# Optimization experiments

Hardware: AMD Instinct MI355X
Metric: run time of the kernel (lower is better)

Reference implementation:

```python
import jax, jax.numpy as jnp
import numpy as np

HIDDEN = 2048
N_HEADS = 32
HEAD_DIM = HIDDEN // N_HEADS  # 64
SEQ = 2048
BATCH = 1
CHUNK = 256
TOPK = 4
THETA = 10000.0
EPS = 1e-6
NEG = jnp.float32(-1e30)


def setup_inputs() -> dict:
    key = jax.random.key(0)
    ks = jax.random.split(key, 8)
    s = 0.02
    return {
        "hidden_states": jax.random.normal(ks[0], (BATCH, SEQ, HIDDEN), jnp.float32),
        "Wq": jax.random.normal(ks[1], (HIDDEN, HIDDEN), jnp.float32) * s,
        "Wk": jax.random.normal(ks[2], (HIDDEN, HIDDEN), jnp.float32) * s,
        "Wv": jax.random.normal(ks[3], (HIDDEN, HIDDEN), jnp.float32) * s,
        "Wo": jax.random.normal(ks[4], (HIDDEN, HIDDEN), jnp.float32) * s,
        "Wg1": jax.random.normal(ks[5], (HEAD_DIM, HIDDEN), jnp.float32) * s,
        "Wg2": jax.random.normal(ks[6], (HIDDEN, HEAD_DIM), jnp.float32) * s,
        "o_norm_weight": jnp.ones((HEAD_DIM,), jnp.float32),
    }


def _rope(t):
    # t: [B, S, H, D]; non-interleaved (NeoX-style) rotary over full head dim
    D = t.shape[-1]
    pos = jnp.arange(t.shape[1], dtype=jnp.float32)
    inv_freq = 1.0 / (THETA ** (jnp.arange(0, D, 2, dtype=jnp.float32) / D))
    freqs = pos[:, None] * inv_freq[None, :]            # [S, D/2]
    cos = jnp.cos(freqs)[None, :, None, :]
    sin = jnp.sin(freqs)[None, :, None, :]
    t1, t2 = t[..., : D // 2], t[..., D // 2:]
    return jnp.concatenate([t1 * cos - t2 * sin, t1 * sin + t2 * cos], axis=-1)


def reference(hidden_states, Wq, Wk, Wv, Wo, Wg1, Wg2, o_norm_weight):
    B, S, _ = hidden_states.shape
    H, D, C = N_HEADS, HEAD_DIM, CHUNK
    NC = S // C

    q = (hidden_states @ Wq.T).reshape(B, S, H, D)
    k = (hidden_states @ Wk.T).reshape(B, S, H, D)
    v = (hidden_states @ Wv.T).reshape(B, S, H, D)
    q, k = _rope(q), _rope(k)

    # --- MoBA gating: per-chunk mean-pooled keys scored against each query ---
    kmean = k.reshape(B, NC, C, H, D).mean(axis=2)           # [B, NC, H, D]
    gate = jnp.einsum('bshd,bnhd->bhsn', q, kmean)           # [B, H, S, NC]

    pos = jnp.arange(S)
    q_chunk = pos // C                                       # [S]
    chunk_ids = jnp.arange(NC)
    future = chunk_ids[None, :] > q_chunk[:, None]           # [S, NC]
    self_blk = chunk_ids[None, :] == q_chunk[:, None]
    gate = jnp.where(future[None, None], NEG, gate)
    gate = jnp.where(self_blk[None, None], -NEG, gate)       # self block always selected

    _, topk_idx = jax.lax.top_k(gate, TOPK)                  # [B, H, S, TOPK]
    sel = jax.nn.one_hot(topk_idx, NC, dtype=jnp.bool_).any(axis=-2)  # [B, H, S, NC]

    # --- block-sparse causal attention over selected chunks ---
    allowed = jnp.take(sel, q_chunk, axis=-1)                # [B, H, S, S] key j -> chunk j//C
    causal = pos[None, :] <= pos[:, None]                    # [S, S]
    allowed = allowed & causal[None, None]

    scale = 1.0 / np.sqrt(D)
    scores = jnp.einsum('bshd,bthd->bhst', q, k) * scale
    scores = jnp.where(allowed, scores, NEG)
    p = jax.nn.softmax(scores, axis=-1)
    o = jnp.einsum('bhst,bthd->bshd', p, v)                  # [B, S, H, D]

    # --- gated RMSNorm (FusedRMSNormGated, sigmoid activation) ---
    g = ((hidden_states @ Wg1.T) @ Wg2.T).reshape(B, S, H, D)
    rms = jax.lax.rsqrt(jnp.mean(o * o, axis=-1, keepdims=True) + EPS)
    o = o * rms * o_norm_weight * jax.nn.sigmoid(g)

    return (o.reshape(B, S, H * D)) @ Wo.T
```

## Files before the change

kernel.cpp:

```cpp
#include <hip/hip_runtime.h>
#include <hip/hip_bf16.h>


typedef __attribute__((ext_vector_type(8))) short s8v;
typedef __attribute__((ext_vector_type(4))) float f4v;

#define MFMA16(A,B,C) __builtin_amdgcn_mfma_f32_16x16x32_bf16(A,B,C,0,0,0)

__device__ __forceinline__ unsigned short f2b_rne(float f){
  unsigned u = __builtin_bit_cast(unsigned, f);
  u = (u + 0x7FFFu + ((u>>16)&1u)) >> 16;
  return (unsigned short)u;
}
__device__ __forceinline__ float b2f(unsigned short h){
  unsigned u = ((unsigned)h)<<16;
  return __builtin_bit_cast(float, u);
}
__device__ __forceinline__ unsigned pack2(float a, float b){
  return (unsigned)f2b_rne(a) | ((unsigned)f2b_rne(b)<<16);
}
__device__ __forceinline__ void gld16(const void* g, void* l){
  __builtin_amdgcn_global_load_lds((const __attribute__((address_space(1))) void*)g,
                                   (__attribute__((address_space(3))) void*)l, 16, 0, 0);
}

__global__ __launch_bounds__(256) void rtab_k(double2* __restrict__ tab){
  const int i = blockIdx.x*256 + threadIdx.x;
  if (i >= 2048*32) return;
  const int d2 = i & 31, s = i >> 5;
  const double invf = 1.0 / pow(10000.0, (double)d2 / 32.0);
  const double ph = (double)s * invf;
  tab[i] = make_double2(cos(ph), sin(ph));
}

__global__ __launch_bounds__(256) void f2b4_k(const float* __restrict__ s,
                                              unsigned short* __restrict__ d, int n4){
  int i = blockIdx.x*256 + threadIdx.x;
  if (i >= n4) return;
  const float4 v = *(const float4*)(s + (size_t)i*4);
  uint2 p; p.x = pack2(v.x, v.y); p.y = pack2(v.z, v.w);
  *(uint2*)(d + (size_t)i*4) = p;
}

__global__ __launch_bounds__(256) void f2bs_k(const float* __restrict__ s,
    unsigned short* __restrict__ hi, unsigned short* __restrict__ lo, int n4){
  int i = blockIdx.x*256 + threadIdx.x;
  if (i >= n4) return;
  const float4 v = *(const float4*)(s + (size_t)i*4);
  unsigned short h0 = f2b_rne(v.x), h1 = f2b_rne(v.y), h2 = f2b_rne(v.z), h3 = f2b_rne(v.w);
  uint2 ph; ph.x = (unsigned)h0 | ((unsigned)h1<<16); ph.y = (unsigned)h2 | ((unsigned)h3<<16);
  uint2 pl; pl.x = pack2(v.x - b2f(h0), v.y - b2f(h1));
  pl.y = pack2(v.z - b2f(h2), v.w - b2f(h3));
  *(uint2*)(hi + (size_t)i*4) = ph;
  *(uint2*)(lo + (size_t)i*4) = pl;
}

__global__ __launch_bounds__(256) void d2bs_k(const double* __restrict__ s,
    unsigned short* __restrict__ hi, unsigned short* __restrict__ lo, int n2){
  const int i = blockIdx.x*256 + threadIdx.x;
  if (i >= n2) return;
  #pragma unroll
  for (int j = 0; j < 2; ++j) {
    const float f = (float)s[(size_t)i*2+j];
    const unsigned short h = f2b_rne(f);
    hi[(size_t)i*2+j] = h;
    lo[(size_t)i*2+j] = f2b_rne(f - b2f(h));
  }
}

__global__ __launch_bounds__(1024) void wsum_k(const float* __restrict__ hs,
    const double2* __restrict__ tab, double* __restrict__ Ac, double* __restrict__ As){
  const int n = blockIdx.x, d2 = blockIdx.y, tid = threadIdx.x;
  double ac0=0, as0=0, ac1=0, as1=0;
  for (int i = 0; i < 256; ++i) {
    const int s = n*256 + i;
    const double2 t = tab[s*32 + d2];
    const double v0 = (double)hs[(size_t)s*2048 + tid];
    const double v1 = (double)hs[(size_t)s*2048 + tid + 1024];
    ac0 += t.x*v0; as0 += t.y*v0;
    ac1 += t.x*v1; as1 += t.y*v1;
  }
  const size_t ro = (size_t)(n*32 + d2)*2048;
  Ac[ro + tid]      = ac0*(1.0/256.0);
  Ac[ro + tid+1024] = ac1*(1.0/256.0);
  As[ro + tid]      = as0*(1.0/256.0);
  As[ro + tid+1024] = as1*(1.0/256.0);
}

__global__ __launch_bounds__(256) void kmcomb_k(const float* __restrict__ Cc,
    const float* __restrict__ Cs, double* __restrict__ Km){
  const int i = blockIdx.x*256 + threadIdx.x;
  const int d = i & 63, h = (i>>6) & 31, n = i >> 11;
  const int d2 = d & 31;
  const size_t row = (size_t)(n*32 + d2)*2048;
  double v;
  if (d < 32) v = (double)Cc[row + h*64 + d2] - (double)Cs[row + h*64 + d2 + 32];
  else        v = (double)Cs[row + h*64 + d2] + (double)Cc[row + h*64 + d2 + 32];
  Km[(size_t)(n*32 + h)*64 + d] = v;
}

__global__ __launch_bounds__(256) void gate_topk_k(const float* __restrict__ Qf,
    const double* __restrict__ Km, unsigned char* __restrict__ Allow,
    unsigned char* __restrict__ Flags){
  const int h = blockIdx.x, c = blockIdx.y, t = threadIdx.x;
  __shared__ double km[512];
  km[t]     = Km[((t>>6)*32 + h)*64 + (t&63)];
  km[t+256] = Km[(((t+256)>>6)*32 + h)*64 + (t&63)];
  __syncthreads();
  const int s = c*256 + t;
  const float* qp = Qf + (size_t)s*2048 + h*64;
  double g[8] = {};
  for (int d = 0; d < 64; ++d) {
    const double qv = (double)qp[d];
    #pragma unroll
    for (int n2 = 0; n2 < 8; ++n2) g[n2] += qv*km[n2*64+d];
  }
  double margin = 1e300;
  if (c >= 4) {
    unsigned pm = 0;
    double v[4];
    for (int rep = 0; rep < 4; ++rep) {
      double best = -1e308; int bi = 0;
      #pragma unroll
      for (int n2 = 0; n2 < 8; ++n2) {
        const bool take = (n2 < c) && !((pm>>n2)&1u) && (g[n2] > best);
        best = take ? g[n2] : best;
        bi   = take ? n2 : bi;
      }
      v[rep] = best; pm |= 1u<<bi;
    }
    margin = v[2] - v[3];
  }
  Flags[h*2048 + s] = (margin < 1e-3) ? 1 : 0;
  #pragma unroll
  for (int n2 = 0; n2 < 8; ++n2) if (n2 > c) g[n2] = -1e300;
  g[c] = 1e300;
  unsigned mask = 0;
  for (int rep = 0; rep < 4; ++rep) {
    double best = -1e308; int bi = 0;
    #pragma unroll
    for (int n2 = 0; n2 < 8; ++n2) {
      const bool take = !((mask>>n2)&1u) && (g[n2] > best);
      best = take ? g[n2] : best;
      bi   = take ? n2 : bi;
    }
    mask |= 1u<<bi;
  }
  Allow[h*2048 + s] = (unsigned char)mask;
}

__global__ __launch_bounds__(64) void repair_k(
    const float* __restrict__ hs, const float* __restrict__ Wq,
    const double2* __restrict__ tab, const double* __restrict__ Km,
    const unsigned char* __restrict__ Flags, unsigned char* __restrict__ Allow)
{
  const int s = blockIdx.x, d = threadIdx.x;
  __shared__ double qr[64];
  __shared__ double g8[8];
  for (int h = 0; h < 32; ++h) {
    if (!Flags[h*2048 + s]) continue;
    const float* hrow = hs + (size_t)s*2048;
    const float* wrow = Wq + (size_t)(h*64 + d)*2048;
    double a0=0,a1=0,a2=0,a3=0;
    for (int k = 0; k < 2048; k += 4) {
      a0 += (double)hrow[k]  *(double)wrow[k];
      a1 += (double)hrow[k+1]*(double)wrow[k+1];
      a2 += (double)hrow[k+2]*(double)wrow[k+2];
      a3 += (double)hrow[k+3]*(double)wrow[k+3];
    }
    qr[d] = (a0+a1)+(a2+a3);
    __syncthreads();
    const double2 t = tab[s*32 + (d&31)];
    const double rot = (d < 32) ? (qr[d]*t.x - qr[d+32]*t.y)
                                : (qr[d-32]*t.y + qr[d]*t.x);
    __syncthreads();
    qr[d] = rot;
    __syncthreads();
    if (d < 8) {
      double g = 0;
      const double* kmp = Km + (size_t)(d*32 + h)*64;
      for (int dd = 0; dd < 64; ++dd) g += qr[dd]*kmp[dd];
      g8[d] = g;
    }
    __syncthreads();
    if (d == 0) {
      const int c = s >> 8;
      double g[8];
      #pragma unroll
      for (int n2 = 0; n2 < 8; ++n2)
        g[n2] = (n2 > c) ? -1e300 : ((n2 == c) ? 1e300 : g8[n2]);
      unsigned mask = 0;
      for (int rep = 0; rep < 4; ++rep) {
        double best = -1e308; int bi = 0;
        #pragma unroll
        for (int n2 = 0; n2 < 8; ++n2) {
          const bool take = !((mask>>n2)&1u) && (g[n2] > best);
          best = take ? g[n2] : best;
          bi   = take ? n2 : bi;
        }
        mask |= 1u<<bi;
      }
      Allow[h*2048 + s] = (unsigned char)mask;
    }
    __syncthreads();
  }
}

__global__ __launch_bounds__(256) void gemm4_bt(
    const unsigned short* __restrict__ Ah, const unsigned short* __restrict__ Al,
    const unsigned short* __restrict__ Bh, const unsigned short* __restrict__ Bl,
    float* __restrict__ C, int M, int N, int K)
{
  alignas(16) __shared__ char SAh[16384];
  alignas(16) __shared__ char SAl[16384];
  alignas(16) __shared__ char SBh[16384];
  alignas(16) __shared__ char SBl[16384];
  const int t = threadIdx.x;
  const int wave = t>>6, lane = t&63, lg = lane>>4, lr = lane&15;
  const int wm = wave >> 1, wn = wave & 1;
  const int m0 = blockIdx.x*128, n0 = blockIdx.y*128;
  const unsigned short* Ahb = Ah + (size_t)m0*K;
  const unsigned short* Alb = Al + (size_t)m0*K;
  const unsigned short* Bhb = Bh + (size_t)n0*K;
  const unsigned short* Blb = Bl + (size_t)n0*K;
  f4v acc[4][4] = {};
  #pragma unroll 1
  for (int kt = 0; kt < K; kt += 64) {
    __syncthreads();
    #pragma unroll
    for (int i = 0; i < 4; ++i) {
      const size_t go = (size_t)(i*32 + (t>>3))*K + kt + (t&7)*8;
      gld16(Ahb + go, SAh + i*4096 + wave*1024);
      gld16(Alb + go, SAl + i*4096 + wave*1024);
      gld16(Bhb + go, SBh + i*4096 + wave*1024);
      gld16(Blb + go, SBl + i*4096 + wave*1024);
    }
    __syncthreads();
    #pragma unroll
    for (int kk = 0; kk < 2; ++kk) {
      s8v ah[4], al[4], bh[4], bl[4];
      #pragma unroll
      for (int i = 0; i < 4; ++i) {
        const int ro = (wm*64 + i*16 + lr)*128 + kk*64 + lg*16;
        ah[i] = *(const s8v*)&SAh[ro];
        al[i] = *(const s8v*)&SAl[ro];
      }
      #pragma unroll
      for (int j = 0; j < 4; ++j) {
        const int ro = (wn*64 + j*16 + lr)*128 + kk*64 + lg*16;
        bh[j] = *(const s8v*)&SBh[ro];
        bl[j] = *(const s8v*)&SBl[ro];
      }
      #pragma unroll
      for (int i = 0; i < 4; ++i)
        #pragma unroll
        for (int j = 0; j < 4; ++j) {
          f4v a = acc[i][j];
          a = MFMA16(ah[i], bh[j], a);
          a = MFMA16(ah[i], bl[j], a);
          a = MFMA16(al[i], bh[j], a);
          a = MFMA16(al[i], bl[j], a);
          acc[i][j] = a;
        }
    }
  }
  #pragma unroll
  for (int i = 0; i < 4; ++i)
    #pragma unroll
    for (int j = 0; j < 4; ++j) {
      const int row = m0 + wm*64 + i*16 + lg*4;
      const int col = n0 + wn*64 + j*16 + lr;
      #pragma unroll
      for (int r = 0; r < 4; ++r)
        C[(size_t)(row+r)*N + col] = acc[i][j][r];
    }
}

template<int BM, int BN, int WN, bool OUTBF>
__global__ __launch_bounds__(256) void gemm_bt(
    const unsigned short* __restrict__ A, const unsigned short* __restrict__ B,
    void* __restrict__ C, int M, int N, int K)
{
  alignas(16) __shared__ char AsB[BM*128];
  alignas(16) __shared__ char BsB[BN*128];
  const int t = threadIdx.x;
  const int wave = t>>6, lane = t&63, lg = lane>>4, lr = lane&15;
  const int wm = wave / WN, wn = wave % WN;
  const int m0 = blockIdx.x*BM, n0 = blockIdx.y*BN;
  const unsigned short* Ab = A + (size_t)m0*K;
  const unsigned short* Bb = B + (size_t)n0*K;
  f4v acc[4][4] = {};
  #pragma unroll 1
  for (int kt = 0; kt < K; kt += 64) {
    __syncthreads();
    #pragma unroll
    for (int i = 0; i < BM/32; ++i)
      gld16(Ab + (size_t)(i*32 + (t>>3))*K + kt + (t&7)*8, AsB + i*4096 + wave*1024);
    #pragma unroll
    for (int i = 0; i < BN/32; ++i)
      gld16(Bb + (size_t)(i*32 + (t>>3))*K + kt + (t&7)*8, BsB + i*4096 + wave*1024);
    __syncthreads();
    #pragma unroll
    for (int kk = 0; kk < 2; ++kk) {
      s8v af[4], bfr[4];
      #pragma unroll
      for (int i = 0; i < 4; ++i)
        af[i] = *(const s8v*)&AsB[(wm*64 + i*16 + lr)*128 + kk*64 + lg*16];
      #pragma unroll
      for (int j = 0; j < 4; ++j)
        bfr[j] = *(const s8v*)&BsB[(wn*64 + j*16 + lr)*128 + kk*64 + lg*16];
      #pragma unroll
      for (int i = 0; i < 4; ++i)
        #pragma unroll
        for (int j = 0; j < 4; ++j)
          acc[i][j] = MFMA16(af[i], bfr[j], acc[i][j]);
    }
  }
  #pragma unroll
  for (int i = 0; i < 4; ++i)
    #pragma unroll
    for (int j = 0; j < 4; ++j) {
      const int row = m0 + wm*64 + i*16 + lg*4;
      const int col = n0 + wn*64 + j*16 + lr;
      #pragma unroll
      for (int r = 0; r < 4; ++r) {
        if (OUTBF) ((unsigned short*)C)[(size_t)(row+r)*N + col] = f2b_rne(acc[i][j][r]);
        else       ((float*)C)[(size_t)(row+r)*N + col] = acc[i][j][r];
      }
    }
}

__global__ __launch_bounds__(256) void rope32q_k(float* __restrict__ Qf,
    unsigned short* __restrict__ Qb, const double2* __restrict__ tab){
  const int idx = blockIdx.x*256 + threadIdx.x;
  const int d2 = idx & 31, hh = (idx>>5)&31, s = idx>>10;
  const double2 t = tab[s*32 + d2];
  const float cs = (float)t.x, sn = (float)t.y;
  const size_t base = (size_t)s*2048 + hh*64 + d2;
  const float q1 = Qf[base], q2 = Qf[base+32];
  const float o1 = q1*cs - q2*sn, o2 = q1*sn + q2*cs;
  Qf[base] = o1; Qf[base+32] = o2;
  Qb[base] = f2b_rne(o1); Qb[base+32] = f2b_rne(o2);
}

__global__ __launch_bounds__(256) void rope32_k(const float* __restrict__ Kf,
    unsigned short* __restrict__ Kb, const double2* __restrict__ tab){
  const int idx = blockIdx.x*256 + threadIdx.x;
  const int d2 = idx & 31, hh = (idx>>5)&31, s = idx>>10;
  const double2 t = tab[s*32 + d2];
  const float cs = (float)t.x, sn = (float)t.y;
  const size_t base = (size_t)s*2048 + hh*64 + d2;
  const float k1 = Kf[base], k2 = Kf[base+32];
  Kb[base]    = f2b_rne(k1*cs - k2*sn);
  Kb[base+32] = f2b_rne(k1*sn + k2*cs);
}

__global__ __launch_bounds__(256) void vtrans_k(const float* __restrict__ V,
                                                unsigned short* __restrict__ Vt){
  __shared__ unsigned short tile[64][68];
  const int s0 = blockIdx.x*64, c0 = blockIdx.y*64;
  const int tx = threadIdx.x & 63, ty = threadIdx.x >> 6;
  #pragma unroll
  for (int rr = 0; rr < 16; ++rr) {
    const int r = ty*16 + rr;
    tile[tx][r] = f2b_rne(V[(size_t)(s0+r)*2048 + c0+tx]);
  }
  __syncthreads();
  #pragma unroll
  for (int rr = 0; rr < 16; ++rr) {
    const int cc = ty*16 + rr;
    Vt[(size_t)(c0+cc)*2048 + s0+tx] = tile[cc][tx];
  }
}

__global__ __launch_bounds__(64) void attn_k(
    const unsigned short* __restrict__ Qb, const unsigned short* __restrict__ Kb,
    const unsigned short* __restrict__ Vt, const float* __restrict__ Gf,
    const unsigned char* __restrict__ Allow, const float* __restrict__ Wn,
    float* __restrict__ Of)
{
  const int h = blockIdx.x, c = blockIdx.y, zb = blockIdx.z;
  const int lane = threadIdx.x, lg = lane>>4, lr = lane&15;
  const int qbase = c*256 + zb*16;
  alignas(16) __shared__ char P[2048];

  const size_t qrow = (size_t)(qbase + lr);
  const s8v qf0 = *(const s8v*)&Qb[qrow*2048 + h*64 + lg*8];
  const s8v qf1 = *(const s8v*)&Qb[qrow*2048 + h*64 + 32 + lg*8];
  const unsigned am = Allow[h*2048 + qrow];
  const int q = qbase + lr;
  const int sw = (lr&7)<<4;

  float mx = -1e30f, ls = 0.f;
  f4v ot[4] = {};

  for (int n = 0; n <= c; ++n) {
    if (!__ballot((am>>n)&1u)) continue;
    const int okc = (am>>n)&1;
    #pragma unroll 1
    for (int t4 = 0; t4 < 4; ++t4) {
      const int kb0 = n*256 + t4*64;
      s8v kf[4][2];
      #pragma unroll
      for (int i = 0; i < 4; ++i) {
        const size_t krow = (size_t)(kb0 + i*16 + lr);
        kf[i][0] = *(const s8v*)&Kb[krow*2048 + h*64 + lg*8];
        kf[i][1] = *(const s8v*)&Kb[krow*2048 + h*64 + 32 + lg*8];
      }
      f4v st[4];
      #pragma unroll
      for (int i = 0; i < 4; ++i) {
        f4v zz = {};
        zz = MFMA16(kf[i][0], qf0, zz);
        st[i] = MFMA16(kf[i][1], qf1, zz);
      }
      float cm = -__builtin_inff();
      #pragma unroll
      for (int i = 0; i < 4; ++i)
        #pragma unroll
        for (int r = 0; r < 4; ++r) {
          float v = st[i][r]*0.125f;
          const int key = kb0 + i*16 + lg*4 + r;
          const bool ok = okc && (n != c || key <= q);
          v = ok ? v : -__builtin_inff();
          st[i][r] = v;
          cm = fmaxf(cm, v);
        }
      cm = fmaxf(cm, __shfl_xor(cm, 16));
      cm = fmaxf(cm, __shfl_xor(cm, 32));
      const float nm = fmaxf(mx, cm);
      const float al = __expf(mx - nm);
      mx = nm;
      float ps = 0.f;
      #pragma unroll
      for (int i = 0; i < 4; ++i) {
        const float p0 = __expf(st[i][0]-mx);
        const float p1 = __expf(st[i][1]-mx);
        const float p2 = __expf(st[i][2]-mx);
        const float p3 = __expf(st[i][3]-mx);
        ps += (p0+p1)+(p2+p3);
        uint2 pk; pk.x = pack2(p0,p1); pk.y = pack2(p2,p3);
        *(uint2*)&P[lr*128 + ((i*32 + lg*8) ^ sw)] = pk;
      }
      ps += __shfl_xor(ps, 16);
      ps += __shfl_xor(ps, 32);
      ls = ls*al + ps;
      #pragma unroll
      for (int jd = 0; jd < 4; ++jd) ot[jd] *= al;
      asm volatile("s_waitcnt lgkmcnt(0)" ::: "memory");
      __builtin_amdgcn_sched_barrier(0);
      #pragma unroll
      for (int kk = 0; kk < 2; ++kk) {
        s8v vfr[4];
        #pragma unroll
        for (int jd = 0; jd < 4; ++jd)
          vfr[jd] = *(const s8v*)&Vt[(size_t)(h*64 + jd*16 + lr)*2048 + kb0 + kk*32 + lg*8];
        const s8v pfr = *(const s8v*)&P[lr*128 + ((kk*64 + lg*16) ^ sw)];
        #pragma unroll
        for (int jd = 0; jd < 4; ++jd)
          ot[jd] = MFMA16(vfr[jd], pfr, ot[jd]);
      }
      asm volatile("s_waitcnt lgkmcnt(0)" ::: "memory");
      __builtin_amdgcn_sched_barrier(0);
    }
  }
  const float inv_ = 1.0f/ls;
  float ssum = 0.f;
  #pragma unroll
  for (int jd = 0; jd < 4; ++jd)
    #pragma unroll
    for (int r = 0; r < 4; ++r) {
      const float o = ot[jd][r]*inv_;
      ot[jd][r] = o;
      ssum += o*o;
    }
  ssum += __shfl_xor(ssum, 16);
  ssum += __shfl_xor(ssum, 32);
  const float rmsv = rsqrtf(ssum*(1.0f/64.0f) + 1e-6f);
  #pragma unroll
  for (int jd = 0; jd < 4; ++jd) {
    const float4 w4 = *(const float4*)&Wn[jd*16 + lg*4];
    const float4 g4 = *(const float4*)&Gf[qrow*2048 + h*64 + jd*16 + lg*4];
    float4 o4;
    o4.x = ot[jd][0]*rmsv*w4.x*(1.0f/(1.0f+__expf(-g4.x)));
    o4.y = ot[jd][1]*rmsv*w4.y*(1.0f/(1.0f+__expf(-g4.y)));
    o4.z = ot[jd][2]*rmsv*w4.z*(1.0f/(1.0f+__expf(-g4.z)));
    o4.w = ot[jd][3]*rmsv*w4.w*(1.0f/(1.0f+__expf(-g4.w)));
    *(float4*)&Of[qrow*2048 + h*64 + jd*16 + lg*4] = o4;
  }
}

extern "C" void kernel_launch(void* const* d_in, const int* in_sizes, int n_in,
                              void* d_out, int out_size, void* d_ws, size_t ws_size,
                              hipStream_t stream)
{
  const float* hs  = (const float*)d_in[0];
  const float* Wq  = (const float*)d_in[1];
  const float* Wk  = (const float*)d_in[2];
  const float* Wv  = (const float*)d_in[3];
  const float* Wo  = (const float*)d_in[4];
  const float* Wg1 = (const float*)d_in[5];
  const float* Wg2 = (const float*)d_in[6];
  const float* Wn  = (const float*)d_in[7];

  const size_t S2 = (size_t)2048*2048;
  const size_t MB = (size_t)1<<20;
  char* ws = (char*)d_ws;
  double2*        tab   = (double2*)       (ws);
  unsigned short* Wg1b  = (unsigned short*)(ws + 1*MB);
  unsigned short* Wg2b  = (unsigned short*)(ws + 1*MB + 262144);
  unsigned short* g1b   = (unsigned short*)(ws + 1*MB + 524288);
  double*         km    = (double*)        (ws + 1*MB + 786432);
  unsigned char*  allow = (unsigned char*) (ws + 1*MB + 917504);
  unsigned char*  flags = (unsigned char*) (ws + 1*MB + 983040);
  unsigned short* hsh   = (unsigned short*)(ws + 2*MB);
  unsigned short* hsl   = (unsigned short*)(ws + 10*MB);
  unsigned short* Wqh   = (unsigned short*)(ws + 18*MB);
  unsigned short* Wql   = (unsigned short*)(ws + 26*MB);
  unsigned short* Wkh   = (unsigned short*)(ws + 34*MB);
  unsigned short* Wkl   = (unsigned short*)(ws + 42*MB);
  unsigned short* Wvb   = (unsigned short*)(ws + 50*MB);
  float*          qf    = (float*)         (ws + 58*MB);
  float*          kf    = (float*)         (ws + 74*MB);
  float*          vf    = (float*)         (ws + 90*MB);
  double*         Ac    = (double*)        (ws + 106*MB);
  double*         As    = (double*)        (ws + 110*MB);
  unsigned short* Ach   = (unsigned short*)(ws + 18*MB);
  unsigned short* Acl   = (unsigned short*)(ws + 19*MB);
  unsigned short* Ash   = (unsigned short*)(ws + 20*MB);
  unsigned short* Asl   = (unsigned short*)(ws + 21*MB);
  float*          Cc    = (float*)         (ws + 22*MB);
  float*          Cs    = (float*)         (ws + 24*MB);
  unsigned short* qb    = (unsigned short*)(ws + 26*MB);
  unsigned short* kb    = (unsigned short*)(ws + 42*MB);
  unsigned short* vt    = (unsigned short*)(ws + 74*MB);
  unsigned short* ofb   = (unsigned short*)(ws + 82*MB);
  float*          gf    = (float*)         (ws + 90*MB);
  float*          of    = (float*)         (ws + 58*MB);
  unsigned short* Wob   = (unsigned short*)(ws + 106*MB);
  (void)ws_size; (void)in_sizes; (void)n_in; (void)out_size;

  rtab_k<<<256,256,0,stream>>>(tab);
  f2bs_k<<<4096,256,0,stream>>>(hs, hsh, hsl, (int)(S2/4));
  f2bs_k<<<4096,256,0,stream>>>(Wq, Wqh, Wql, (int)(S2/4));
  f2bs_k<<<4096,256,0,stream>>>(Wk, Wkh, Wkl, (int)(S2/4));
  f2b4_k<<<4096,256,0,stream>>>(Wv, Wvb, (int)(S2/4));
  f2b4_k<<<128,256,0,stream>>>(Wg1, Wg1b, 64*2048/4);
  f2b4_k<<<128,256,0,stream>>>(Wg2, Wg2b, 2048*64/4);

  gemm4_bt<<<dim3(16,16),256,0,stream>>>(hsh, hsl, Wqh, Wql, qf, 2048, 2048, 2048);
  gemm_bt<128,128,2,false><<<dim3(16,16),256,0,stream>>>(hsh, Wkh, kf, 2048, 2048, 2048);
  gemm_bt<128,128,2,false><<<dim3(16,16),256,0,stream>>>(hsh, Wvb, vf, 2048, 2048, 2048);

  rope32q_k<<<8192,256,0,stream>>>(qf, qb, tab);

  wsum_k<<<dim3(8,32),1024,0,stream>>>(hs, tab, Ac, As);
  d2bs_k<<<1024,256,0,stream>>>(Ac, Ach, Acl, 262144);
  d2bs_k<<<1024,256,0,stream>>>(As, Ash, Asl, 262144);
  gemm4_bt<<<dim3(2,16),256,0,stream>>>(Ach, Acl, Wkh, Wkl, Cc, 256, 2048, 2048);
  gemm4_bt<<<dim3(2,16),256,0,stream>>>(Ash, Asl, Wkh, Wkl, Cs, 256, 2048, 2048);
  kmcomb_k<<<64,256,0,stream>>>(Cc, Cs, km);

  rope32_k<<<8192,256,0,stream>>>(kf, kb, tab);

  gate_topk_k<<<dim3(32,8),256,0,stream>>>(qf, km, allow, flags);
  repair_k<<<2048,64,0,stream>>>(hs, Wq, tab, km, flags, allow);

  vtrans_k<<<dim3(32,32),256,0,stream>>>(vf, vt);
  gemm_bt<256,64,1,true><<<dim3(8,1),256,0,stream>>>(hsh, Wg1b, g1b, 2048, 64, 2048);
  gemm_bt<128,128,2,false><<<dim3(16,16),256,0,stream>>>(g1b, Wg2b, gf, 2048, 2048, 64);

  attn_k<<<dim3(32,8,16),64,0,stream>>>(qb, kb, vt, gf, allow, Wn, of);

  f2b4_k<<<4096,256,0,stream>>>(of, ofb, (int)(S2/4));
  f2b4_k<<<4096,256,0,stream>>>(Wo, Wob, (int)(S2/4));
  gemm_bt<128,128,2,false><<<dim3(16,16),256,0,stream>>>(ofb, Wob, d_out, 2048, 2048, 2048);
}
```

Before: 850.4 us.

## Software-pipeline K loads with double buffering and hoist V loads in sparse attention

Restructures the block-sparse attention loop to precompute a bitmask of active chunks and iterate over them directly. K fragments for the next 64-key tile, including the first tile of the next active chunk, are prefetched into alternating register buffers while the current tile is computed. V fragments are now loaded at the start of each tile rather than after the softmax, so global-load latency can overlap the QK MFMAs and the softmax. The cost is higher register pressure from the extra K buffer and the hoisted V fragments, which may reduce occupancy.

Result: no change. 837.1 us (-1.6%).

```diff
diff --git a/kernel.cpp b/kernel.cpp
--- a/kernel.cpp
+++ b/kernel.cpp
@@ -394,74 +394,97 @@
   float mx = -1e30f, ls = 0.f;
   f4v ot[4] = {};
 
-  for (int n = 0; n <= c; ++n) {
-    if (!__ballot((am>>n)&1u)) continue;
-    const int okc = (am>>n)&1;
-    #pragma unroll 1
-    for (int t4 = 0; t4 < 4; ++t4) {
-      const int kb0 = n*256 + t4*64;
-      s8v kf[4][2];
-      #pragma unroll
-      for (int i = 0; i < 4; ++i) {
-        const size_t krow = (size_t)(kb0 + i*16 + lr);
-        kf[i][0] = *(const s8v*)&Kb[krow*2048 + h*64 + lg*8];
-        kf[i][1] = *(const s8v*)&Kb[krow*2048 + h*64 + 32 + lg*8];
+  unsigned act = 0;
+  for (int n = 0; n <= c; ++n)
+    if (__ballot((am>>n)&1u)) act |= (1u<<n);
+
+  auto loadK = [&](s8v (&kf)[4][2], int kb0){
+    #pragma unroll
+    for (int i = 0; i < 4; ++i) {
+      const size_t krow = (size_t)(kb0 + i*16 + lr);
+      kf[i][0] = *(const s8v*)&Kb[krow*2048 + h*64 + lg*8];
+      kf[i][1] = *(const s8v*)&Kb[krow*2048 + h*64 + 32 + lg*8];
+    }
+  };
+
+  if (act) {
+    int n = (int)__builtin_ctz(act);
+    s8v kA[4][2], kB[4][2];
+    loadK(kA, n*256);
+    while (true) {
+      const unsigned rem = (n >= 31) ? 0u : (act & ~((2u << n) - 1u));
+      const int nnext = rem ? (int)__builtin_ctz(rem) : -1;
+      const int okc = (am>>n)&1;
+      #pragma unroll
+      for (int t4 = 0; t4 < 4; ++t4) {
+        const int kb0 = n*256 + t4*64;
+        if (t4 < 3) {
+          if (t4 & 1) loadK(kA, kb0 + 64);
+          else        loadK(kB, kb0 + 64);
+        } else if (nnext >= 0) {
+          loadK(kA, nnext*256);
+        }
+        s8v vfr[2][4];
+        #pragma unroll
+        for (int kk = 0; kk < 2; ++kk)
+          #pragma unroll
+          for (int jd = 0; jd < 4; ++jd)
+            vfr[kk][jd] = *(const s8v*)&Vt[(size_t)(h*64 + jd*16 + lr)*2048 + kb0 + kk*32 + lg*8];
+        const s8v (*kc)[2] = (t4 & 1) ? kB : kA;
+        f4v st[4];
+        #pragma unroll
+        for (int i = 0; i < 4; ++i) {
+          f4v zz = {};
+          zz = MFMA16(kc[i][0], qf0, zz);
+          st[i] = MFMA16(kc[i][1], qf1, zz);
+        }
+        float cm = -__builtin_inff();
+        #pragma unroll
+        for (int i = 0; i < 4; ++i)
+          #pragma unroll
+          for (int r = 0; r < 4; ++r) {
+            float v = st[i][r]*0.125f;
+            const int key = kb0 + i*16 + lg*4 + r;
+            const bool ok = okc && (n != c || key <= q);
+            v = ok ? v : -__builtin_inff();
+            st[i][r] = v;
+            cm = fmaxf(cm, v);
+          }
+        cm = fmaxf(cm, __shfl_xor(cm, 16));
+        cm = fmaxf(cm, __shfl_xor(cm, 32));
+        const float nm = fmaxf(mx, cm);
+        const float al = __expf(mx - nm);
+        mx = nm;
+        float ps = 0.f;
+        #pragma unroll
+        for (int i = 0; i < 4; ++i) {
+          const float p0 = __expf(st[i][0]-mx);
+          const float p1 = __expf(st[i][1]-mx);
+          const float p2 = __expf(st[i][2]-mx);
+          const float p3 = __expf(st[i][3]-mx);
+          ps += (p0+p1)+(p2+p3);
+          uint2 pk; pk.x = pack2(p0,p1); pk.y = pack2(p2,p3);
+          *(uint2*)&P[lr*128 + ((i*32 + lg*8) ^ sw)] = pk;
+        }
+        ps += __shfl_xor(ps, 16);
+        ps += __shfl_xor(ps, 32);
+        ls = ls*al + ps;
+        #pragma unroll
+        for (int jd = 0; jd < 4; ++jd) ot[jd] *= al;
+        asm volatile("s_waitcnt lgkmcnt(0)" ::: "memory");
+        __builtin_amdgcn_sched_barrier(0);
+        #pragma unroll
+        for (int kk = 0; kk < 2; ++kk) {
+          const s8v pfr = *(const s8v*)&P[lr*128 + ((kk*64 + lg*16) ^ sw)];
+          #pragma unroll
+          for (int jd = 0; jd < 4; ++jd)
+            ot[jd] = MFMA16(vfr[kk][jd], pfr, ot[jd]);
+        }
+        asm volatile("s_waitcnt lgkmcnt(0)" ::: "memory");
+        __builtin_amdgcn_sched_barrier(0);
       }
-      f4v st[4];
-      #pragma unroll
-      for (int i = 0; i < 4; ++i) {
-        f4v zz = {};
-        zz = MFMA16(kf[i][0], qf0, zz);
-        st[i] = MFMA16(kf[i][1], qf1, zz);
-      }
-      float cm = -__builtin_inff();
-      #pragma unroll
-      for (int i = 0; i < 4; ++i)
-        #pragma unroll
-        for (int r = 0; r < 4; ++r) {
-          float v = st[i][r]*0.125f;
-          const int key = kb0 + i*16 + lg*4 + r;
-          const bool ok = okc && (n != c || key <= q);
-          v = ok ? v : -__builtin_inff();
-          st[i][r] = v;
-          cm = fmaxf(cm, v);
-        }
-      cm = fmaxf(cm, __shfl_xor(cm, 16));
-      cm = fmaxf(cm, __shfl_xor(cm, 32));
-      const float nm = fmaxf(mx, cm);
-      const float al = __expf(mx - nm);
-      mx = nm;
-      float ps = 0.f;
-      #pragma unroll
-      for (int i = 0; i < 4; ++i) {
-        const float p0 = __expf(st[i][0]-mx);
-        const float p1 = __expf(st[i][1]-mx);
-        const float p2 = __expf(st[i][2]-mx);
-        const float p3 = __expf(st[i][3]-mx);
-        ps += (p0+p1)+(p2+p3);
-        uint2 pk; pk.x = pack2(p0,p1); pk.y = pack2(p2,p3);
-        *(uint2*)&P[lr*128 + ((i*32 + lg*8) ^ sw)] = pk;
-      }
-      ps += __shfl_xor(ps, 16);
-      ps += __shfl_xor(ps, 32);
-      ls = ls*al + ps;
-      #pragma unroll
-      for (int jd = 0; jd < 4; ++jd) ot[jd] *= al;
-      asm volatile("s_waitcnt lgkmcnt(0)" ::: "memory");
-      __builtin_amdgcn_sched_barrier(0);
-      #pragma unroll
-      for (int kk = 0; kk < 2; ++kk) {
-        s8v vfr[4];
-        #pragma unroll
-        for (int jd = 0; jd < 4; ++jd)
-          vfr[jd] = *(const s8v*)&Vt[(size_t)(h*64 + jd*16 + lr)*2048 + kb0 + kk*32 + lg*8];
-        const s8v pfr = *(const s8v*)&P[lr*128 + ((kk*64 + lg*16) ^ sw)];
-        #pragma unroll
-        for (int jd = 0; jd < 4; ++jd)
-          ot[jd] = MFMA16(vfr[jd], pfr, ot[jd]);
-      }
-      asm volatile("s_waitcnt lgkmcnt(0)" ::: "memory");
-      __builtin_amdgcn_sched_barrier(0);
+      if (nnext < 0) break;
+      n = nnext;
     }
   }
   const float inv_ = 1.0f/ls;
```
